# Kernel tuning notes

Hardware: AMD Instinct MI355X
Metric: run time of the kernel (lower is better)

Reference implementation:

```python
import jax, jax.numpy as jnp
import numpy as np

N_NODES, N_EDGES, H_DIM = 100000, 1000000, 64
NUM_RELS, NUM_BASES, N_HID = 32, 4, 2


def setup_inputs() -> dict:
    key = jax.random.key(0)
    ks = jax.random.split(key, 8)
    features = jax.random.normal(ks[0], (N_NODES, H_DIM), dtype=jnp.float32)
    norm = jax.random.uniform(ks[1], (N_EDGES, 1), dtype=jnp.float32)
    # basis-decomposition params per layer: V [L,B,D,D], comp [L,R,B], bias [L,D]
    V = jax.random.normal(ks[2], (N_HID, NUM_BASES, H_DIM, H_DIM), dtype=jnp.float32) * 0.05
    comp = jax.random.normal(ks[3], (N_HID, NUM_RELS, NUM_BASES), dtype=jnp.float32)
    bias = jnp.zeros((N_HID, H_DIM), dtype=jnp.float32)
    src = jax.random.randint(ks[4], (N_EDGES,), 0, N_NODES, dtype=jnp.int32)
    dst = jax.random.randint(ks[5], (N_EDGES,), 0, N_NODES, dtype=jnp.int32)
    edge_type = jax.random.randint(ks[6], (N_EDGES,), 0, NUM_RELS, dtype=jnp.int32)
    return {"features": features, "norm": norm, "V": V, "comp": comp,
            "bias": bias, "src": src, "dst": dst, "edge_type": edge_type}


def rel_graph_conv(x, V_l, comp_l, bias_l, src, dst, edge_type, norm, num_nodes):
    # project nodes through all bases first (cheap: N*B*D*D), then gather per edge
    xb = jnp.einsum('ni,bio->nbo', x, V_l)          # [N, B, D]
    coef = comp_l[edge_type]                         # [E, B] per-edge relation coeffs
    msg = jnp.einsum('eb,ebo->eo', coef, xb[src])    # [E, D]
    msg = msg * norm                                 # per-edge norm [E,1]
    h = jax.ops.segment_sum(msg, dst, num_segments=num_nodes)  # [N, D]
    return h + bias_l


def reference(features, norm, V, comp, bias, src, dst, edge_type):
    num_nodes = features.shape[0]
    skip = features
    x = features
    # faithful to source: every layer reads the ORIGINAL `features`;
    # only the last layer's output survives (x overwritten each iteration)
    for l in range(V.shape[0]):
        h = rel_graph_conv(features, V[l], comp[l], bias[l],
                           src, dst, edge_type, norm, num_nodes)
        x = jax.nn.relu(h)
    return x + skip
```

## Files before the change

kernel.cpp:

```cpp
#include <hip/hip_runtime.h>

#define HD   64
#define NB   4
#define MAXDEG 64
#define BNODES 1024
#define BCAP   16384

typedef __attribute__((ext_vector_type(8))) short bf16x8;
typedef __attribute__((ext_vector_type(4))) float f32x4;
typedef __attribute__((ext_vector_type(2))) float f2v;

__device__ __forceinline__ unsigned short f2bf(float f) {
    union { float f; unsigned int i; } c; c.f = f;
    unsigned int r = c.i + 0x7FFF + ((c.i >> 16) & 1);
    return (unsigned short)(r >> 16);
}
__device__ __forceinline__ unsigned int pack2(float a, float b) {
    return (unsigned)f2bf(a) | ((unsigned)f2bf(b) << 16);
}
__device__ __forceinline__ float lo_bf(unsigned int w) {
    union { unsigned int i; float f; } c; c.i = w << 16; return c.f;
}
__device__ __forceinline__ float hi_bf(unsigned int w) {
    union { unsigned int i; float f; } c; c.i = w & 0xFFFF0000u; return c.f;
}

__global__ __launch_bounds__(256) void binfb_kernel(
    const int* __restrict__ dst, const int* __restrict__ src,
    const int* __restrict__ etype, const float* __restrict__ norm,
    int* __restrict__ gcursor, uint2* __restrict__ binned, int n_edges,
    const float* __restrict__ Vl, unsigned short* __restrict__ vpack,
    const float* __restrict__ f, unsigned short* __restrict__ fb, int n_nodes,
    int binblocks, int fbblocks, int nbuck) {
    __shared__ uint2 srec[2048];
    __shared__ unsigned char sbid[2048];
    __shared__ int lcnt[128];
    __shared__ int lscan[128];
    __shared__ int lstart[128];
    __shared__ int gbase[128];
    long long tot = binblocks + fbblocks;
    int t = threadIdx.x;
    if ((long long)blockIdx.x == tot) {
#pragma unroll
        for (int i = 0; i < 8; ++i) {
            int s = t + i * 256;
            int lane = s & 63;
            int ctks = s >> 6;
            int ks = ctks & 7, ct = ctks >> 3;
            int o = ct * 16 + (lane & 15);
            unsigned int w[4];
#pragma unroll
            for (int j = 0; j < 4; ++j) {
                int k0 = ks * 32 + ((lane >> 4) & 3) * 8 + 2 * j;
                w[j] = pack2(Vl[(size_t)k0 * HD + o], Vl[(size_t)(k0 + 1) * HD + o]);
            }
            *(uint4*)(vpack + (size_t)s * 8) = make_uint4(w[0], w[1], w[2], w[3]);
        }
        return;
    }
    long long i = blockIdx.x;
    int bin_before = (int)((i * binblocks) / tot);
    int bin_after  = (int)(((i + 1) * binblocks) / tot);
    if (bin_after == bin_before) {
        int gid = ((int)i - bin_before) * 256 + t;
        long long base = (long long)gid * 8;
        long long total = (long long)n_nodes * HD;
        if (base + 7 < total) {
            float4 v0 = *(const float4*)(f + base);
            float4 v1 = *(const float4*)(f + base + 4);
            uint4 p = make_uint4(pack2(v0.x, v0.y), pack2(v0.z, v0.w),
                                 pack2(v1.x, v1.y), pack2(v1.z, v1.w));
            ((uint4*)fb)[gid] = p;
        }
        return;
    }
    int base = bin_before * 2048;
    if (t < 128) lcnt[t] = 0;
    __syncthreads();
    int b8[8], lr[8];
#pragma unroll
    for (int j = 0; j < 8; ++j) {
        int e = base + j * 256 + t;
        if (e < n_edges) {
            b8[j] = dst[e] >> 10;
            lr[j] = atomicAdd(&lcnt[b8[j]], 1);
        } else b8[j] = -1;
    }
    __syncthreads();
    if (t < 128) lscan[t] = lcnt[t];
    __syncthreads();
    for (int off2 = 1; off2 < 128; off2 <<= 1) {
        int x = 0;
        if (t < 128 && t >= off2) x = lscan[t - off2];
        __syncthreads();
        if (t < 128) lscan[t] += x;
        __syncthreads();
    }
    if (t < 128) lstart[t] = lscan[t] - lcnt[t];
    if (t < nbuck) {
        int c = lcnt[t];
        gbase[t] = c ? atomicAdd(&gcursor[t], c) : 0;
    }
    __syncthreads();
#pragma unroll
    for (int j = 0; j < 8; ++j) {
        if (b8[j] < 0) continue;
        int e = base + j * 256 + t;
        int d = dst[e];
        int ld = d & (BNODES - 1);
        uint2 rr;
        rr.x = (unsigned)src[e] | ((unsigned)etype[e] << 20)
             | ((unsigned)(ld & 0x7F) << 25);
        rr.y = (__float_as_uint(norm[e]) & ~7u) | (unsigned)(ld >> 7);
        int slot = lstart[b8[j]] + lr[j];
        srec[slot] = rr;
        sbid[slot] = (unsigned char)b8[j];
    }
    __syncthreads();
    int nvalid = n_edges - base; if (nvalid > 2048) nvalid = 2048;
    for (int s2 = t; s2 < nvalid; s2 += 256) {
        int b = sbid[s2];
        int pos = gbase[b] + (s2 - lstart[b]);
        if (pos < BCAP) binned[(size_t)b * BCAP + pos] = srec[s2];
    }
}

__global__ __launch_bounds__(1024) void bsort_kernel(
    const uint2* __restrict__ binned, const int* __restrict__ gcursor,
    uint2* __restrict__ rec, int* __restrict__ cnt, int n_nodes) {
    __shared__ int lcnt[BNODES];
    int b = blockIdx.x;
    int t = threadIdx.x;
    lcnt[t] = 0;
    __syncthreads();
    int nb = gcursor[b]; if (nb > BCAP) nb = BCAP;
    const uint2* bb = binned + (size_t)b * BCAP;
    for (int i = t; i < nb; i += 1024) {
        uint2 q = bb[i];
        int ld = (int)((q.x >> 25) & 0x7F) | ((int)(q.y & 7u) << 7);
        int lr = atomicAdd(&lcnt[ld], 1);
        if (lr < MAXDEG)
            rec[((size_t)b * BNODES + ld) * MAXDEG + lr] = q;
    }
    __syncthreads();
    int dn = b * BNODES + t;
    if (dn < n_nodes) cnt[dn] = lcnt[t];
}

#define G_STRIDE_U32 132
__global__ __launch_bounds__(256) void aggproj_kernel(
    const uint2* __restrict__ rec, const int* __restrict__ cnt,
    const unsigned int* __restrict__ fb32,
    const float* __restrict__ comp_l, const float* __restrict__ bias_l,
    const float* __restrict__ f, float* __restrict__ out,
    const unsigned short* __restrict__ vpack, int n_nodes, int n_rels) {
    __shared__ unsigned int glds[16 * G_STRIDE_U32];
    __shared__ float4 comp_s[32];
    int t = threadIdx.x;
    if (t < n_rels) comp_s[t] = ((const float4*)comp_l)[t];
    __syncthreads();

    int l32 = t & 31;
    int halfbase = t & 32;
    int hw = t >> 5;
    int wv = t >> 6;
    int d0 = blockIdx.x * 16;

#pragma unroll
    for (int ss = 0; ss < 2; ++ss) {
        int n = hw + ss * 8;
        int d = d0 + n;
        f2v a0 = {0.f, 0.f}, a1 = {0.f, 0.f}, a2 = {0.f, 0.f}, a3 = {0.f, 0.f};
        if (d < n_nodes) {
            int deg = cnt[d];
            if (deg > MAXDEG) deg = MAXDEG;
            size_t start = (size_t)d * MAXDEG;
            for (int cb = 0; cb < deg; cb += 32) {
                int m = deg - cb; if (m > 32) m = 32;
                uint2 myq = make_uint2(0u, 0u);
                if (cb + l32 < deg) myq = rec[start + cb + l32];
                int j = 0;
                for (; j + 3 < m; j += 4) {
                    unsigned qx0 = __shfl(myq.x, halfbase + j,     64);
                    unsigned qy0 = __shfl(myq.y, halfbase + j,     64);
                    unsigned qx1 = __shfl(myq.x, halfbase + j + 1, 64);
                    unsigned qy1 = __shfl(myq.y, halfbase + j + 1, 64);
                    unsigned qx2 = __shfl(myq.x, halfbase + j + 2, 64);
                    unsigned qy2 = __shfl(myq.y, halfbase + j + 2, 64);
                    unsigned qx3 = __shfl(myq.x, halfbase + j + 3, 64);
                    unsigned qy3 = __shfl(myq.y, halfbase + j + 3, 64);
                    unsigned fw0 = fb32[(size_t)(qx0 & 0xFFFFF) * 32 + l32];
                    unsigned fw1 = fb32[(size_t)(qx1 & 0xFFFFF) * 32 + l32];
                    unsigned fw2 = fb32[(size_t)(qx2 & 0xFFFFF) * 32 + l32];
                    unsigned fw3 = fb32[(size_t)(qx3 & 0xFFFFF) * 32 + l32];
                    float4 c0 = comp_s[(qx0 >> 20) & 31];
                    float4 c1 = comp_s[(qx1 >> 20) & 31];
                    float4 c2 = comp_s[(qx2 >> 20) & 31];
                    float4 c3 = comp_s[(qx3 >> 20) & 31];
                    float nn0 = __uint_as_float(qy0 & ~7u), nn1 = __uint_as_float(qy1 & ~7u);
                    float nn2 = __uint_as_float(qy2 & ~7u), nn3 = __uint_as_float(qy3 & ~7u);
                    f2v f01;
                    f01 = (f2v){lo_bf(fw0), hi_bf(fw0)};
                    a0 += f01 * (nn0 * c0.x); a1 += f01 * (nn0 * c0.y);
                    a2 += f01 * (nn0 * c0.z); a3 += f01 * (nn0 * c0.w);
                    f01 = (f2v){lo_bf(fw1), hi_bf(fw1)};
                    a0 += f01 * (nn1 * c1.x); a1 += f01 * (nn1 * c1.y);
                    a2 += f01 * (nn1 * c1.z); a3 += f01 * (nn1 * c1.w);
                    f01 = (f2v){lo_bf(fw2), hi_bf(fw2)};
                    a0 += f01 * (nn2 * c2.x); a1 += f01 * (nn2 * c2.y);
                    a2 += f01 * (nn2 * c2.z); a3 += f01 * (nn2 * c2.w);
                    f01 = (f2v){lo_bf(fw3), hi_bf(fw3)};
                    a0 += f01 * (nn3 * c3.x); a1 += f01 * (nn3 * c3.y);
                    a2 += f01 * (nn3 * c3.z); a3 += f01 * (nn3 * c3.w);
                }
                for (; j < m; ++j) {
                    unsigned qx = __shfl(myq.x, halfbase + j, 64);
                    unsigned qy = __shfl(myq.y, halfbase + j, 64);
                    unsigned fw = fb32[(size_t)(qx & 0xFFFFF) * 32 + l32];
                    float4 c = comp_s[(qx >> 20) & 31];
                    float nn = __uint_as_float(qy & ~7u);
                    f2v f01 = (f2v){lo_bf(fw), hi_bf(fw)};
                    a0 += f01 * (nn * c.x); a1 += f01 * (nn * c.y);
                    a2 += f01 * (nn * c.z); a3 += f01 * (nn * c.w);
                }
            }
        }
        glds[n * G_STRIDE_U32 + 0 * 32 + l32] = pack2(a0[0], a0[1]);
        glds[n * G_STRIDE_U32 + 1 * 32 + l32] = pack2(a1[0], a1[1]);
        glds[n * G_STRIDE_U32 + 2 * 32 + l32] = pack2(a2[0], a2[1]);
        glds[n * G_STRIDE_U32 + 3 * 32 + l32] = pack2(a3[0], a3[1]);
    }
    __syncthreads();

    int lane = t & 63;
    int row = lane & 15;
    int hi = (lane >> 4) & 3;
    int ct = wv;
    f32x4 acc = (f32x4){0.f, 0.f, 0.f, 0.f};
#pragma unroll
    for (int ks = 0; ks < 8; ++ks) {
        bf16x8 bfrag = *reinterpret_cast<const bf16x8*>(
            (const char*)glds + row * (G_STRIDE_U32 * 4) + ks * 64 + hi * 16);
        bf16x8 afrag = *reinterpret_cast<const bf16x8*>(
            vpack + ((size_t)(ct * 8 + ks) * 64 + lane) * 8);
        acc = __builtin_amdgcn_mfma_f32_16x16x32_bf16(afrag, bfrag, acc, 0, 0, 0);
    }
    int dst_n = d0 + row;
    if (dst_n < n_nodes) {
        int o0 = ct * 16 + hi * 4;
        float4 b4 = *(const float4*)(bias_l + o0);
        float4 fv = *(const float4*)(f + (size_t)dst_n * HD + o0);
        float4 res;
        res.x = fmaxf(acc[0] + b4.x, 0.f) + fv.x;
        res.y = fmaxf(acc[1] + b4.y, 0.f) + fv.y;
        res.z = fmaxf(acc[2] + b4.z, 0.f) + fv.z;
        res.w = fmaxf(acc[3] + b4.w, 0.f) + fv.w;
        *(float4*)(out + (size_t)dst_n * HD + o0) = res;
    }
}

extern "C" void kernel_launch(void* const* d_in, const int* in_sizes, int n_in,
                              void* d_out, int out_size, void* d_ws, size_t ws_size,
                              hipStream_t stream) {
    const float* features = (const float*)d_in[0];
    const float* norm     = (const float*)d_in[1];
    const float* V        = (const float*)d_in[2];
    const float* comp     = (const float*)d_in[3];
    const float* bias     = (const float*)d_in[4];
    const int*   src      = (const int*)d_in[5];
    const int*   dst      = (const int*)d_in[6];
    const int*   etype    = (const int*)d_in[7];
    float* out = (float*)d_out;

    int n_nodes = in_sizes[0] / HD;
    int n_edges = in_sizes[5];
    int L       = in_sizes[2] / (NB * HD * HD);
    int l       = L - 1;
    int comp_stride = in_sizes[3] / L;
    int n_rels  = comp_stride / NB;

    const float* Vl     = V    + (size_t)l * NB * HD * HD;
    const float* comp_l = comp + (size_t)l * comp_stride;
    const float* bias_l = bias + (size_t)l * HD;

    int nbuck = (n_nodes + BNODES - 1) / BNODES;

    char* ws = (char*)d_ws;
    size_t off = 0;
    unsigned short* fb = (unsigned short*)(ws + off); off += (size_t)n_nodes * HD * sizeof(unsigned short);
    off = (off + 15) & ~(size_t)15;
    int* cnt     = (int*)(ws + off);  off += (size_t)n_nodes * sizeof(int);
    int* gcursor = (int*)(ws + off);  off += 128 * sizeof(int);
    unsigned short* vpack = (unsigned short*)(ws + off); off += 2048 * 8 * sizeof(unsigned short);
    off = (off + 15) & ~(size_t)15;
    uint2* binned = (uint2*)(ws + off); off += (size_t)nbuck * BCAP * sizeof(uint2);
    uint2* rec    = (uint2*)(ws + off);

    hipMemsetAsync(gcursor, 0, 128 * sizeof(int), stream);

    int binblocks = (n_edges + 2047) / 2048;
    long long total_el = (long long)n_nodes * HD;
    int fbblocks = (int)((total_el + 2047) / 2048);

    binfb_kernel<<<binblocks + fbblocks + 1, 256, 0, stream>>>(
        dst, src, etype, norm, gcursor, binned, n_edges,
        Vl, vpack, features, fb, n_nodes, binblocks, fbblocks, nbuck);

    bsort_kernel<<<nbuck, 1024, 0, stream>>>(binned, gcursor, rec, cnt, n_nodes);

    aggproj_kernel<<<(n_nodes + 15) / 16, 256, 0, stream>>>(
        rec, cnt, (const unsigned int*)fb, comp_l, bias_l, features, out,
        vpack, n_nodes, n_rels);
}
```

Baseline: 84.72 us.

## Split bucket sort across sub-blocks and process 32 nodes per aggproj block

The bucket sort kernel now runs each bucket with four sub-blocks. Each sub-block counts its chunk in shared memory and reserves slots with global atomics on cnt, which is now zeroed by a larger memset. This is meant to raise parallelism over roughly 98 large blocks. The aggregation/projection kernel now handles 32 destination nodes per block with two MFMA row groups, reusing the V fragments, and the per-edge coefficient scaling is vectorized. The sort assumes each sub-block chunk fits in 4×1024 entries (BCAP 16384 / 4), and edge order within a node is now nondeterministic.

```diff
diff --git a/kernel.cpp b/kernel.cpp
--- a/kernel.cpp
+++ b/kernel.cpp
@@ -5,6 +5,8 @@
 #define MAXDEG 64
 #define BNODES 1024
 #define BCAP   16384
+#define SUBB 4
+#define DPB  32
 
 typedef __attribute__((ext_vector_type(8))) short bf16x8;
 typedef __attribute__((ext_vector_type(4))) float f32x4;
@@ -129,22 +131,41 @@
     const uint2* __restrict__ binned, const int* __restrict__ gcursor,
     uint2* __restrict__ rec, int* __restrict__ cnt, int n_nodes) {
     __shared__ int lcnt[BNODES];
-    int b = blockIdx.x;
+    __shared__ int lbase[BNODES];
+    int b = blockIdx.x / SUBB;
+    int sb = blockIdx.x - b * SUBB;
     int t = threadIdx.x;
     lcnt[t] = 0;
     __syncthreads();
     int nb = gcursor[b]; if (nb > BCAP) nb = BCAP;
+    int chunk = (nb + SUBB - 1) / SUBB;
+    int lo = sb * chunk;
+    int hi = lo + chunk; if (hi > nb) hi = nb;
     const uint2* bb = binned + (size_t)b * BCAP;
-    for (int i = t; i < nb; i += 1024) {
-        uint2 q = bb[i];
-        int ld = (int)((q.x >> 25) & 0x7F) | ((int)(q.y & 7u) << 7);
-        int lr = atomicAdd(&lcnt[ld], 1);
-        if (lr < MAXDEG)
-            rec[((size_t)b * BNODES + ld) * MAXDEG + lr] = q;
-    }
-    __syncthreads();
-    int dn = b * BNODES + t;
-    if (dn < n_nodes) cnt[dn] = lcnt[t];
+    uint2 q[4]; int ld[4], lr[4];
+#pragma unroll
+    for (int k = 0; k < 4; ++k) {
+        int idx = lo + k * 1024 + t;
+        if (idx < hi) {
+            q[k] = bb[idx];
+            ld[k] = (int)((q[k].x >> 25) & 0x7F) | ((int)(q[k].y & 7u) << 7);
+            lr[k] = atomicAdd(&lcnt[ld[k]], 1);
+        } else ld[k] = -1;
+    }
+    __syncthreads();
+    {
+        int c = lcnt[t];
+        int dn = b * BNODES + t;
+        lbase[t] = (c && dn < n_nodes) ? atomicAdd(&cnt[dn], c) : 0;
+    }
+    __syncthreads();
+#pragma unroll
+    for (int k = 0; k < 4; ++k) {
+        if (ld[k] < 0) continue;
+        int r = lbase[ld[k]] + lr[k];
+        if (r < MAXDEG)
+            rec[((size_t)b * BNODES + ld[k]) * MAXDEG + r] = q[k];
+    }
 }
 
 #define G_STRIDE_U32 132
@@ -154,7 +175,7 @@
     const float* __restrict__ comp_l, const float* __restrict__ bias_l,
     const float* __restrict__ f, float* __restrict__ out,
     const unsigned short* __restrict__ vpack, int n_nodes, int n_rels) {
-    __shared__ unsigned int glds[16 * G_STRIDE_U32];
+    __shared__ unsigned int glds[DPB * G_STRIDE_U32];
     __shared__ float4 comp_s[32];
     int t = threadIdx.x;
     if (t < n_rels) comp_s[t] = ((const float4*)comp_l)[t];
@@ -164,10 +185,10 @@
     int halfbase = t & 32;
     int hw = t >> 5;
     int wv = t >> 6;
-    int d0 = blockIdx.x * 16;
-
-#pragma unroll
-    for (int ss = 0; ss < 2; ++ss) {
+    int d0 = blockIdx.x * DPB;
+
+#pragma unroll
+    for (int ss = 0; ss < DPB / 8; ++ss) {
         int n = hw + ss * 8;
         int d = d0 + n;
         f2v a0 = {0.f, 0.f}, a1 = {0.f, 0.f}, a2 = {0.f, 0.f}, a3 = {0.f, 0.f};
@@ -199,19 +220,23 @@
                     float4 c3 = comp_s[(qx3 >> 20) & 31];
                     float nn0 = __uint_as_float(qy0 & ~7u), nn1 = __uint_as_float(qy1 & ~7u);
                     float nn2 = __uint_as_float(qy2 & ~7u), nn3 = __uint_as_float(qy3 & ~7u);
-                    f2v f01;
+                    f2v f01, wA, wB;
                     f01 = (f2v){lo_bf(fw0), hi_bf(fw0)};
-                    a0 += f01 * (nn0 * c0.x); a1 += f01 * (nn0 * c0.y);
-                    a2 += f01 * (nn0 * c0.z); a3 += f01 * (nn0 * c0.w);
+                    wA = (f2v){c0.x, c0.y} * nn0; wB = (f2v){c0.z, c0.w} * nn0;
+                    a0 += f01 * wA[0]; a1 += f01 * wA[1];
+                    a2 += f01 * wB[0]; a3 += f01 * wB[1];
                     f01 = (f2v){lo_bf(fw1), hi_bf(fw1)};
-                    a0 += f01 * (nn1 * c1.x); a1 += f01 * (nn1 * c1.y);
-                    a2 += f01 * (nn1 * c1.z); a3 += f01 * (nn1 * c1.w);
+                    wA = (f2v){c1.x, c1.y} * nn1; wB = (f2v){c1.z, c1.w} * nn1;
+                    a0 += f01 * wA[0]; a1 += f01 * wA[1];
+                    a2 += f01 * wB[0]; a3 += f01 * wB[1];
                     f01 = (f2v){lo_bf(fw2), hi_bf(fw2)};
-                    a0 += f01 * (nn2 * c2.x); a1 += f01 * (nn2 * c2.y);
-                    a2 += f01 * (nn2 * c2.z); a3 += f01 * (nn2 * c2.w);
+                    wA = (f2v){c2.x, c2.y} * nn2; wB = (f2v){c2.z, c2.w} * nn2;
+                    a0 += f01 * wA[0]; a1 += f01 * wA[1];
+                    a2 += f01 * wB[0]; a3 += f01 * wB[1];
                     f01 = (f2v){lo_bf(fw3), hi_bf(fw3)};
-                    a0 += f01 * (nn3 * c3.x); a1 += f01 * (nn3 * c3.y);
-                    a2 += f01 * (nn3 * c3.z); a3 += f01 * (nn3 * c3.w);
+                    wA = (f2v){c3.x, c3.y} * nn3; wB = (f2v){c3.z, c3.w} * nn3;
+                    a0 += f01 * wA[0]; a1 += f01 * wA[1];
+                    a2 += f01 * wB[0]; a3 += f01 * wB[1];
                 }
                 for (; j < m; ++j) {
                     unsigned qx = __shfl(myq.x, halfbase + j, 64);
@@ -220,8 +245,10 @@
                     float4 c = comp_s[(qx >> 20) & 31];
                     float nn = __uint_as_float(qy & ~7u);
                     f2v f01 = (f2v){lo_bf(fw), hi_bf(fw)};
-                    a0 += f01 * (nn * c.x); a1 += f01 * (nn * c.y);
-                    a2 += f01 * (nn * c.z); a3 += f01 * (nn * c.w);
+                    f2v wA = (f2v){c.x, c.y} * nn;
+                    f2v wB = (f2v){c.z, c.w} * nn;
+                    a0 += f01 * wA[0]; a1 += f01 * wA[1];
+                    a2 += f01 * wB[0]; a3 += f01 * wB[1];
                 }
             }
         }
@@ -234,28 +261,31 @@
 
     int lane = t & 63;
     int row = lane & 15;
-    int hi = (lane >> 4) & 3;
+    int hq = (lane >> 4) & 3;
     int ct = wv;
-    f32x4 acc = (f32x4){0.f, 0.f, 0.f, 0.f};
-#pragma unroll
-    for (int ks = 0; ks < 8; ++ks) {
-        bf16x8 bfrag = *reinterpret_cast<const bf16x8*>(
-            (const char*)glds + row * (G_STRIDE_U32 * 4) + ks * 64 + hi * 16);
-        bf16x8 afrag = *reinterpret_cast<const bf16x8*>(
-            vpack + ((size_t)(ct * 8 + ks) * 64 + lane) * 8);
-        acc = __builtin_amdgcn_mfma_f32_16x16x32_bf16(afrag, bfrag, acc, 0, 0, 0);
-    }
-    int dst_n = d0 + row;
-    if (dst_n < n_nodes) {
-        int o0 = ct * 16 + hi * 4;
-        float4 b4 = *(const float4*)(bias_l + o0);
-        float4 fv = *(const float4*)(f + (size_t)dst_n * HD + o0);
-        float4 res;
-        res.x = fmaxf(acc[0] + b4.x, 0.f) + fv.x;
-        res.y = fmaxf(acc[1] + b4.y, 0.f) + fv.y;
-        res.z = fmaxf(acc[2] + b4.z, 0.f) + fv.z;
-        res.w = fmaxf(acc[3] + b4.w, 0.f) + fv.w;
-        *(float4*)(out + (size_t)dst_n * HD + o0) = res;
+#pragma unroll
+    for (int rg = 0; rg < DPB / 16; ++rg) {
+        f32x4 acc = (f32x4){0.f, 0.f, 0.f, 0.f};
+#pragma unroll
+        for (int ks = 0; ks < 8; ++ks) {
+            bf16x8 bfrag = *reinterpret_cast<const bf16x8*>(
+                (const char*)glds + (rg * 16 + row) * (G_STRIDE_U32 * 4) + ks * 64 + hq * 16);
+            bf16x8 afrag = *reinterpret_cast<const bf16x8*>(
+                vpack + ((size_t)(ct * 8 + ks) * 64 + lane) * 8);
+            acc = __builtin_amdgcn_mfma_f32_16x16x32_bf16(afrag, bfrag, acc, 0, 0, 0);
+        }
+        int dst_n = d0 + rg * 16 + row;
+        if (dst_n < n_nodes) {
+            int o0 = ct * 16 + hq * 4;
+            float4 b4 = *(const float4*)(bias_l + o0);
+            float4 fv = *(const float4*)(f + (size_t)dst_n * HD + o0);
+            float4 res;
+            res.x = fmaxf(acc[0] + b4.x, 0.f) + fv.x;
+            res.y = fmaxf(acc[1] + b4.y, 0.f) + fv.y;
+            res.z = fmaxf(acc[2] + b4.z, 0.f) + fv.z;
+            res.w = fmaxf(acc[3] + b4.w, 0.f) + fv.w;
+            *(float4*)(out + (size_t)dst_n * HD + o0) = res;
+        }
     }
 }
 
@@ -296,7 +326,7 @@
     uint2* binned = (uint2*)(ws + off); off += (size_t)nbuck * BCAP * sizeof(uint2);
     uint2* rec    = (uint2*)(ws + off);
 
-    hipMemsetAsync(gcursor, 0, 128 * sizeof(int), stream);
+    hipMemsetAsync(cnt, 0, ((size_t)n_nodes + 128) * sizeof(int), stream);
 
     int binblocks = (n_edges + 2047) / 2048;
     long long total_el = (long long)n_nodes * HD;
@@ -306,9 +336,9 @@
         dst, src, etype, norm, gcursor, binned, n_edges,
         Vl, vpack, features, fb, n_nodes, binblocks, fbblocks, nbuck);
 
-    bsort_kernel<<<nbuck, 1024, 0, stream>>>(binned, gcursor, rec, cnt, n_nodes);
-
-    aggproj_kernel<<<(n_nodes + 15) / 16, 256, 0, stream>>>(
+    bsort_kernel<<<nbuck * SUBB, 1024, 0, stream>>>(binned, gcursor, rec, cnt, n_nodes);
+
+    aggproj_kernel<<<(n_nodes + DPB - 1) / DPB, 256, 0, stream>>>(
         rec, cnt, (const unsigned int*)fb, comp_l, bias_l, features, out,
         vpack, n_nodes, n_rels);
 }
```

Measured after the change: 80.99 us. -4.4%, faster.
